# Optimization experiments

Measured on AMD Instinct MI355X. Metric: run time of the kernel, lower is better.

## Reference

```python
import jax, jax.numpy as jnp
import numpy as np

E, H, VOCAB = 32, 128, 32000
B, T = 32, 128


def _linear_params(key, out_f, in_f):
    kw, kb = jax.random.split(key)
    bound = 1.0 / np.sqrt(in_f)
    W = jax.random.uniform(kw, (out_f, in_f), jnp.float32, -bound, bound)
    b = jax.random.uniform(kb, (out_f,), jnp.float32, -bound, bound)
    return W, b


def setup_inputs() -> dict:
    key = jax.random.key(0)
    ks = jax.random.split(key, 10)
    x = jax.random.normal(ks[0], (B, T, E), jnp.float32)
    Wf, bWf = _linear_params(ks[1], H, E)
    Uf, bUf = _linear_params(ks[2], H, H)
    Wi, bWi = _linear_params(ks[3], H, E)
    Ui, bUi = _linear_params(ks[4], H, H)
    Wc, bWc = _linear_params(ks[5], H, E)
    Uc, bUc = _linear_params(ks[6], H, H)
    Wo, bWo = _linear_params(ks[7], H, E)
    Uo, bUo = _linear_params(ks[8], H, H)
    Vw, Vb = _linear_params(ks[9], VOCAB, H)
    return dict(x=x, Wf=Wf, bWf=bWf, Uf=Uf, bUf=bUf, Wi=Wi, bWi=bWi,
                Ui=Ui, bUi=bUi, Wc=Wc, bWc=bWc, Uc=Uc, bUc=bUc,
                Wo=Wo, bWo=bWo, Uo=Uo, bUo=bUo, Vw=Vw, Vb=Vb)


def _lstm_forward(x, Wf, bWf, Uf, bUf, Wi, bWi, Ui, bUi, Wc, bWc, Uc, bUc,
                  Wo, bWo, Uo, bUo, Vw, Vb):
    b = x.shape[0]
    # Precompute input-to-gate projections for all timesteps: [T, B, H] (time-major)
    xf = (jnp.einsum('bte,he->bth', x, Wf) + bWf).transpose(1, 0, 2)
    xi = (jnp.einsum('bte,he->bth', x, Wi) + bWi).transpose(1, 0, 2)
    xc = (jnp.einsum('bte,he->bth', x, Wc) + bWc).transpose(1, 0, 2)
    xo = (jnp.einsum('bte,he->bth', x, Wo) + bWo).transpose(1, 0, 2)

    h0 = jnp.zeros((b, H), x.dtype)
    c0 = jnp.zeros((b, H), x.dtype)

    def step(carry, xs):
        h, c = carry
        xf_t, xi_t, xc_t, xo_t = xs
        f = jax.nn.sigmoid(xf_t + h @ Uf.T + bUf)
        i = jax.nn.sigmoid(xi_t + h @ Ui.T + bUi)
        c_til = jnp.tanh(xc_t + h @ Uc.T + bUc)
        # Original module detaches the cell state before using it (self.ct = ct.detach())
        c_new = jax.lax.stop_gradient(f * c + i * c_til)
        o = jax.nn.sigmoid(xo_t + h @ Uo.T + bUo)
        h_new = o * jnp.tanh(c_new)
        out = h_new @ Vw.T + Vb  # [B, VOCAB]
        return (h_new, c_new), out

    (h_last, _), outs = jax.lax.scan(step, (h0, c0), (xf, xi, xc, xo))
    out_seq = outs.transpose(1, 0, 2)  # [B, T, VOCAB]
    return out_seq, h_last


def reference(x, Wf, bWf, Uf, bUf, Wi, bWi, Ui, bUi, Wc, bWc, Uc, bUc,
              Wo, bWo, Uo, bUo, Vw, Vb):
    return _lstm_forward(x, Wf, bWf, Uf, bUf, Wi, bWi, Ui, bUi, Wc, bWc,
                         Uc, bUc, Wo, bWo, Uo, bUo, Vw, Vb)
```

## Files before the change

kernel.cpp:

```cpp
#include <hip/hip_runtime.h>
#include <stdint.h>
#include <stddef.h>
#include <math.h>

#define E_ 32
#define H_ 128
#define V_ 32000
#define NB 32
#define NT 128
#define NCONS 224
#define NCHUNK 250
#define NX (NCHUNK - NCONS)
#define WSTEPS 16
#define NWIN (NT / WSTEPS)

typedef float f32x4 __attribute__((ext_vector_type(4)));
typedef short s16x8 __attribute__((ext_vector_type(8)));

__device__ inline unsigned short f2bf(float f) {
  uint32_t u = __float_as_uint(f);
  return (unsigned short)((u + 0x7FFFu + ((u >> 16) & 1u)) >> 16);
}

__global__ void zero_cnt(int* cnt) {
  if (threadIdx.x < NWIN) cnt[threadIdx.x] = 0;
}

__global__ __launch_bounds__(512, 1)
void lstm_fused(const float* __restrict__ x,
                const float* __restrict__ Wf, const float* __restrict__ bWf,
                const float* __restrict__ Uf, const float* __restrict__ bUf,
                const float* __restrict__ Wi, const float* __restrict__ bWi,
                const float* __restrict__ Ui, const float* __restrict__ bUi,
                const float* __restrict__ Wc, const float* __restrict__ bWc,
                const float* __restrict__ Uc, const float* __restrict__ bUc,
                const float* __restrict__ Wo, const float* __restrict__ bWo,
                const float* __restrict__ Uo, const float* __restrict__ bUo,
                const float* __restrict__ Vw, const float* __restrict__ Vb,
                unsigned short* __restrict__ hbf,
                int* __restrict__ cnt,
                float* __restrict__ out,
                float* __restrict__ hlast)
{
  __shared__ __align__(16) unsigned char smem[81920];
  const int bid = blockIdx.x;
  const int tid = threadIdx.x;

  if (bid < NB) {
    float* xs = reinterpret_cast<float*>(smem);
    float* hd = reinterpret_cast<float*>(smem + 16384);

    const int q  = tid & 3;
    const int jj = tid >> 2;

    const float* WL[4]  = {Wf, Wi, Wc, Wo};
    const float* UL[4]  = {Uf, Ui, Uc, Uo};
    const float* bWL[4] = {bWf, bWi, bWc, bWo};
    const float* bUL[4] = {bUf, bUi, bUc, bUo};

    f32x4 wr_[4][2];
    f32x4 ur_[4][8];
    float bias_[4];
#pragma unroll
    for (int g = 0; g < 4; ++g) {
      const f32x4* Wp = reinterpret_cast<const f32x4*>(WL[g] + jj * E_ + q * 8);
      wr_[g][0] = Wp[0]; wr_[g][1] = Wp[1];
      const f32x4* Up = reinterpret_cast<const f32x4*>(UL[g] + jj * H_ + q * 32);
#pragma unroll
      for (int r = 0; r < 8; ++r) ur_[g][r] = Up[r];
      bias_[g] = bWL[g][jj] + bUL[g][jj];
    }

    for (int i = tid; i < NT * E_; i += 512) xs[i] = x[bid * (NT * E_) + i];
    if (tid < 144) hd[tid] = 0.f;
    float creg = 0.f;
    __syncthreads();

    for (int t = 0; t < NT; ++t) {
      const int cur = t & 1, nxt = cur ^ 1;
      const f32x4* hq = reinterpret_cast<const f32x4*>(hd + cur * 144 + q * 36);
      const f32x4* xq = reinterpret_cast<const f32x4*>(xs + t * E_ + q * 8);

      f32x4 p0 = {0.f,0.f,0.f,0.f}, p1 = p0, p2 = p0, p3 = p0;
#pragma unroll
      for (int r = 0; r < 2; ++r) {
        f32x4 xv = xq[r];
        p0 += wr_[0][r] * xv; p1 += wr_[1][r] * xv;
        p2 += wr_[2][r] * xv; p3 += wr_[3][r] * xv;
      }
#pragma unroll
      for (int r = 0; r < 8; ++r) {
        f32x4 hv = hq[r];
        p0 += ur_[0][r] * hv; p1 += ur_[1][r] * hv;
        p2 += ur_[2][r] * hv; p3 += ur_[3][r] * hv;
      }
      float s0 = (p0.x + p0.y) + (p0.z + p0.w);
      float s1 = (p1.x + p1.y) + (p1.z + p1.w);
      float s2 = (p2.x + p2.y) + (p2.z + p2.w);
      float s3 = (p3.x + p3.y) + (p3.z + p3.w);
      s0 += __shfl_xor(s0, 1); s0 += __shfl_xor(s0, 2);
      s1 += __shfl_xor(s1, 1); s1 += __shfl_xor(s1, 2);
      s2 += __shfl_xor(s2, 1); s2 += __shfl_xor(s2, 2);
      s3 += __shfl_xor(s3, 1); s3 += __shfl_xor(s3, 2);
      s0 += bias_[0]; s1 += bias_[1]; s2 += bias_[2]; s3 += bias_[3];

      float own = (q == 0) ? s0 : (q == 1) ? s1 : (q == 2) ? s2 : s3;
      float xin = (q == 2) ? own + own : own;
      float sig = 1.f / (1.f + expf(-xin));
      float val = (q == 2) ? 2.f * sig - 1.f : sig;
      float v1 = __shfl_xor(val, 1);
      float v2 = __shfl_xor(val, 2);
      float v3 = __shfl_xor(v1, 2);
      float f_ = (q == 0) ? val : (q == 1) ? v1 : (q == 2) ? v2 : v3;
      float i_ = (q == 0) ? v1 : (q == 1) ? val : (q == 2) ? v3 : v2;
      float c_ = (q == 0) ? v2 : (q == 1) ? v3 : (q == 2) ? val : v1;
      float o_ = (q == 0) ? v3 : (q == 1) ? v2 : (q == 2) ? v1 : val;

      float cn = f_ * creg + i_ * c_;
      creg = cn;
      float hn = o_ * tanhf(cn);

      if (q == 0) {
        hd[nxt * 144 + jj + ((jj >> 5) << 2)] = hn;
        hbf[((size_t)t * NB + bid) * H_ + jj] = f2bf(hn);
        if (t == NT - 1) hlast[bid * H_ + jj] = hn;
      }
      __syncthreads();
      if ((t & (WSTEPS - 1)) == (WSTEPS - 1) && tid == 0)
        __hip_atomic_fetch_add(&cnt[t / WSTEPS], 1, __ATOMIC_RELEASE,
                               __HIP_MEMORY_SCOPE_AGENT);
    }
    return;
  }

  const int cid = bid - NB;
  unsigned char* vwo = smem;
  unsigned char* vwx = smem + 32768;
  unsigned char* hlb = smem + 65536;

  const int w = tid >> 6, lane = tid & 63;
  const int wr = w & 1, wc = w >> 1;
  const int l15 = lane & 15, lh = lane >> 4;

  for (int u = tid; u < 2048; u += 512) {
    int n = u >> 4, kc = u & 15;
    const f32x4* src = reinterpret_cast<const f32x4*>(
        Vw + ((size_t)(cid * 128 + n)) * H_ + kc * 8);
    f32x4 a = src[0], b = src[1];
    s16x8 o;
    o[0] = (short)f2bf(a.x); o[1] = (short)f2bf(a.y);
    o[2] = (short)f2bf(a.z); o[3] = (short)f2bf(a.w);
    o[4] = (short)f2bf(b.x); o[5] = (short)f2bf(b.y);
    o[6] = (short)f2bf(b.z); o[7] = (short)f2bf(b.w);
    *reinterpret_cast<s16x8*>(vwo + n * 256 + ((kc * 16) ^ ((n & 7) << 4))) = o;
  }
  float vbo0 = Vb[cid * 128 + wc * 32 + l15];
  float vbo1 = Vb[cid * 128 + wc * 32 + 16 + l15];
  const int hb_ = tid >> 4, hkc_ = tid & 15;
  const int hswz = hb_ * 256 + ((hkc_ * 16) ^ ((hb_ & 7) << 4));
  __syncthreads();

  for (int win = 0; win < NWIN; ++win) {
    if (tid == 0) {
      while (__hip_atomic_load(&cnt[win], __ATOMIC_RELAXED,
                               __HIP_MEMORY_SCOPE_AGENT) < NB)
        __builtin_amdgcn_s_sleep(8);
      (void)__hip_atomic_load(&cnt[win], __ATOMIC_ACQUIRE,
                              __HIP_MEMORY_SCOPE_AGENT);
    }
    __syncthreads();

    s16x8 hv = *reinterpret_cast<const s16x8*>(
        hbf + (size_t)(win * WSTEPS) * (NB * H_) + tid * 8);

    const int k = cid - NX * win;
    const bool duty = (k >= 0) && (k < NX);
    int chunk_x = NCONS + k;
    float vbx0 = 0.f, vbx1 = 0.f;
    if (duty) {
      for (int u = tid; u < 2048; u += 512) {
        int n = u >> 4, kc = u & 15;
        const f32x4* src = reinterpret_cast<const f32x4*>(
            Vw + ((size_t)(chunk_x * 128 + n)) * H_ + kc * 8);
        f32x4 a = src[0], b = src[1];
        s16x8 o;
        o[0] = (short)f2bf(a.x); o[1] = (short)f2bf(a.y);
        o[2] = (short)f2bf(a.z); o[3] = (short)f2bf(a.w);
        o[4] = (short)f2bf(b.x); o[5] = (short)f2bf(b.y);
        o[6] = (short)f2bf(b.z); o[7] = (short)f2bf(b.w);
        *reinterpret_cast<s16x8*>(vwx + n * 256 + ((kc * 16) ^ ((n & 7) << 4))) = o;
      }
      vbx0 = Vb[chunk_x * 128 + wc * 32 + l15];
      vbx1 = Vb[chunk_x * 128 + wc * 32 + 16 + l15];
    }

    for (int tt = 0; tt < WSTEPS; ++tt) {
      const int t = win * WSTEPS + tt;
      unsigned char* hcur = hlb + (tt & 1) * 8192;
      *reinterpret_cast<s16x8*>(hcur + hswz) = hv;
      if (tt < WSTEPS - 1)
        hv = *reinterpret_cast<const s16x8*>(
            hbf + (size_t)(t + 1) * (NB * H_) + tid * 8);
      __syncthreads();

      s16x8 af[4];
      const int ra = wr * 16 + l15;
#pragma unroll
      for (int kt = 0; kt < 4; ++kt)
        af[kt] = *reinterpret_cast<const s16x8*>(
            hcur + ra * 256 + ((kt * 64 + lh * 16) ^ ((ra & 7) << 4)));

      const int rb = wc * 32 + l15;
      {
        f32x4 acc0 = {0.f,0.f,0.f,0.f}, acc1 = acc0;
#pragma unroll
        for (int kt = 0; kt < 4; ++kt) {
          s16x8 b0 = *reinterpret_cast<const s16x8*>(
              vwo + rb * 256 + ((kt * 64 + lh * 16) ^ ((rb & 7) << 4)));
          s16x8 b1 = *reinterpret_cast<const s16x8*>(
              vwo + (rb + 16) * 256 + ((kt * 64 + lh * 16) ^ (((rb + 16) & 7) << 4)));
          acc0 = __builtin_amdgcn_mfma_f32_16x16x32_bf16(af[kt], b0, acc0, 0, 0, 0);
          acc1 = __builtin_amdgcn_mfma_f32_16x16x32_bf16(af[kt], b1, acc1, 0, 0, 0);
        }
        const int colbase = cid * 128 + wc * 32;
#pragma unroll
        for (int i = 0; i < 4; ++i) {
          int b = wr * 16 + lh * 4 + i;
          float* orow = out + ((size_t)b * NT + t) * V_ + colbase;
          orow[l15]      = acc0[i] + vbo0;
          orow[16 + l15] = acc1[i] + vbo1;
        }
      }
      if (duty) {
        f32x4 acc0 = {0.f,0.f,0.f,0.f}, acc1 = acc0;
#pragma unroll
        for (int kt = 0; kt < 4; ++kt) {
          s16x8 b0 = *reinterpret_cast<const s16x8*>(
              vwx + rb * 256 + ((kt * 64 + lh * 16) ^ ((rb & 7) << 4)));
          s16x8 b1 = *reinterpret_cast<const s16x8*>(
              vwx + (rb + 16) * 256 + ((kt * 64 + lh * 16) ^ (((rb + 16) & 7) << 4)));
          acc0 = __builtin_amdgcn_mfma_f32_16x16x32_bf16(af[kt], b0, acc0, 0, 0, 0);
          acc1 = __builtin_amdgcn_mfma_f32_16x16x32_bf16(af[kt], b1, acc1, 0, 0, 0);
        }
        const int colbase = chunk_x * 128 + wc * 32;
#pragma unroll
        for (int i = 0; i < 4; ++i) {
          int b = wr * 16 + lh * 4 + i;
          float* orow = out + ((size_t)b * NT + t) * V_ + colbase;
          orow[l15]      = acc0[i] + vbx0;
          orow[16 + l15] = acc1[i] + vbx1;
        }
      }
    }
  }
}

extern "C" void kernel_launch(void* const* d_in, const int* in_sizes, int n_in,
                              void* d_out, int out_size, void* d_ws, size_t ws_size,
                              hipStream_t stream) {
  const float* x   = (const float*)d_in[0];
  const float* Wf  = (const float*)d_in[1];
  const float* bWf = (const float*)d_in[2];
  const float* Uf  = (const float*)d_in[3];
  const float* bUf = (const float*)d_in[4];
  const float* Wi  = (const float*)d_in[5];
  const float* bWi = (const float*)d_in[6];
  const float* Ui  = (const float*)d_in[7];
  const float* bUi = (const float*)d_in[8];
  const float* Wc  = (const float*)d_in[9];
  const float* bWc = (const float*)d_in[10];
  const float* Uc  = (const float*)d_in[11];
  const float* bUc = (const float*)d_in[12];
  const float* Wo  = (const float*)d_in[13];
  const float* bWo = (const float*)d_in[14];
  const float* Uo  = (const float*)d_in[15];
  const float* bUo = (const float*)d_in[16];
  const float* Vw  = (const float*)d_in[17];
  const float* Vb  = (const float*)d_in[18];
  float* out = (float*)d_out;

  unsigned short* hbf = (unsigned short*)d_ws;
  int* cnt = (int*)((char*)d_ws + (1u << 20));
  float* hlast = out + (size_t)NB * NT * V_;

  hipLaunchKernelGGL(zero_cnt, dim3(1), dim3(64), 0, stream, cnt);
  hipLaunchKernelGGL(lstm_fused, dim3(256), dim3(512), 0, stream,
                     x, Wf, bWf, Uf, bUf, Wi, bWi, Ui, bUi, Wc, bWc, Uc, bUc,
                     Wo, bWo, Uo, bUo, Vw, Vb, hbf, cnt, out, hlast);
}
```

Baseline: 190.8 us.

## Double block size to 1024 threads and restructure recurrence and vocab-projection work split

Raises the workgroup size from 512 to 1024 threads. In the recurrent blocks each (hidden unit, gate) pair now gets its own pair of threads instead of four threads per unit, and fast exp/rcp intrinsics replace expf and tanhf. The bf16 h output is staged in shared memory and written once per 16-step window as packed words. In the projection blocks each wave now owns 16 output columns with one MFMA chain instead of 32, so there are more waves in flight. The aim is to shorten the serial per-step critical path and raise MFMA/store parallelism, at the cost of more register pressure at 1024 threads and small accuracy changes from the fast intrinsics.

```diff
diff --git a/kernel.cpp b/kernel.cpp
--- a/kernel.cpp
+++ b/kernel.cpp
@@ -26,7 +26,7 @@
   if (threadIdx.x < NWIN) cnt[threadIdx.x] = 0;
 }
 
-__global__ __launch_bounds__(512, 1)
+__global__ __launch_bounds__(1024, 1)
 void lstm_fused(const float* __restrict__ x,
                 const float* __restrict__ Wf, const float* __restrict__ bWf,
                 const float* __restrict__ Uf, const float* __restrict__ bUf,
@@ -47,87 +47,100 @@
   const int tid = threadIdx.x;
 
   if (bid < NB) {
-    float* xs = reinterpret_cast<float*>(smem);
-    float* hd = reinterpret_cast<float*>(smem + 16384);
-
-    const int q  = tid & 3;
-    const int jj = tid >> 2;
+    float* xs  = reinterpret_cast<float*>(smem);
+    float* hd  = reinterpret_cast<float*>(smem + 16384);
+    float* hfl = reinterpret_cast<float*>(smem + 17408);
+
+    const int j  = tid >> 3;
+    const int g  = (tid >> 1) & 3;
+    const int q2 = tid & 1;
 
     const float* WL[4]  = {Wf, Wi, Wc, Wo};
     const float* UL[4]  = {Uf, Ui, Uc, Uo};
     const float* bWL[4] = {bWf, bWi, bWc, bWo};
     const float* bUL[4] = {bUf, bUi, bUc, bUo};
 
-    f32x4 wr_[4][2];
-    f32x4 ur_[4][8];
-    float bias_[4];
-#pragma unroll
-    for (int g = 0; g < 4; ++g) {
-      const f32x4* Wp = reinterpret_cast<const f32x4*>(WL[g] + jj * E_ + q * 8);
-      wr_[g][0] = Wp[0]; wr_[g][1] = Wp[1];
-      const f32x4* Up = reinterpret_cast<const f32x4*>(UL[g] + jj * H_ + q * 32);
-#pragma unroll
-      for (int r = 0; r < 8; ++r) ur_[g][r] = Up[r];
-      bias_[g] = bWL[g][jj] + bUL[g][jj];
-    }
-
-    for (int i = tid; i < NT * E_; i += 512) xs[i] = x[bid * (NT * E_) + i];
-    if (tid < 144) hd[tid] = 0.f;
+    f32x4 ur_[16];
+    f32x4 wr_[4];
+    {
+      const f32x4* Up = reinterpret_cast<const f32x4*>(UL[g] + j * H_ + q2 * 64);
+#pragma unroll
+      for (int r = 0; r < 16; ++r) ur_[r] = Up[r];
+      const f32x4* Wp = reinterpret_cast<const f32x4*>(WL[g] + j * E_ + q2 * 16);
+#pragma unroll
+      for (int r = 0; r < 4; ++r) wr_[r] = Wp[r];
+    }
+    const float bias = bWL[g][j] + bUL[g][j];
+
+    for (int i = tid; i < NT * E_; i += 1024) xs[i] = x[bid * (NT * E_) + i];
+    if (tid < 128) { hd[tid] = 0.f; hd[128 + tid] = 0.f; }
     float creg = 0.f;
     __syncthreads();
 
-    for (int t = 0; t < NT; ++t) {
-      const int cur = t & 1, nxt = cur ^ 1;
-      const f32x4* hq = reinterpret_cast<const f32x4*>(hd + cur * 144 + q * 36);
-      const f32x4* xq = reinterpret_cast<const f32x4*>(xs + t * E_ + q * 8);
-
-      f32x4 p0 = {0.f,0.f,0.f,0.f}, p1 = p0, p2 = p0, p3 = p0;
-#pragma unroll
-      for (int r = 0; r < 2; ++r) {
-        f32x4 xv = xq[r];
-        p0 += wr_[0][r] * xv; p1 += wr_[1][r] * xv;
-        p2 += wr_[2][r] * xv; p3 += wr_[3][r] * xv;
-      }
-#pragma unroll
-      for (int r = 0; r < 8; ++r) {
-        f32x4 hv = hq[r];
-        p0 += ur_[0][r] * hv; p1 += ur_[1][r] * hv;
-        p2 += ur_[2][r] * hv; p3 += ur_[3][r] * hv;
-      }
-      float s0 = (p0.x + p0.y) + (p0.z + p0.w);
-      float s1 = (p1.x + p1.y) + (p1.z + p1.w);
-      float s2 = (p2.x + p2.y) + (p2.z + p2.w);
-      float s3 = (p3.x + p3.y) + (p3.z + p3.w);
-      s0 += __shfl_xor(s0, 1); s0 += __shfl_xor(s0, 2);
-      s1 += __shfl_xor(s1, 1); s1 += __shfl_xor(s1, 2);
-      s2 += __shfl_xor(s2, 1); s2 += __shfl_xor(s2, 2);
-      s3 += __shfl_xor(s3, 1); s3 += __shfl_xor(s3, 2);
-      s0 += bias_[0]; s1 += bias_[1]; s2 += bias_[2]; s3 += bias_[3];
-
-      float own = (q == 0) ? s0 : (q == 1) ? s1 : (q == 2) ? s2 : s3;
-      float xin = (q == 2) ? own + own : own;
-      float sig = 1.f / (1.f + expf(-xin));
-      float val = (q == 2) ? 2.f * sig - 1.f : sig;
-      float v1 = __shfl_xor(val, 1);
-      float v2 = __shfl_xor(val, 2);
-      float v3 = __shfl_xor(v1, 2);
-      float f_ = (q == 0) ? val : (q == 1) ? v1 : (q == 2) ? v2 : v3;
-      float i_ = (q == 0) ? v1 : (q == 1) ? val : (q == 2) ? v3 : v2;
-      float c_ = (q == 0) ? v2 : (q == 1) ? v3 : (q == 2) ? val : v1;
-      float o_ = (q == 0) ? v3 : (q == 1) ? v2 : (q == 2) ? v1 : val;
-
-      float cn = f_ * creg + i_ * c_;
-      creg = cn;
-      float hn = o_ * tanhf(cn);
-
-      if (q == 0) {
-        hd[nxt * 144 + jj + ((jj >> 5) << 2)] = hn;
-        hbf[((size_t)t * NB + bid) * H_ + jj] = f2bf(hn);
-        if (t == NT - 1) hlast[bid * H_ + jj] = hn;
+    for (int win = 0; win < NWIN; ++win) {
+      for (int tt = 0; tt < WSTEPS; ++tt) {
+        const int t = win * WSTEPS + tt;
+        const int cur = t & 1, nxt = cur ^ 1;
+        const f32x4* hq = reinterpret_cast<const f32x4*>(hd + cur * 128 + q2 * 64);
+        const f32x4* xq = reinterpret_cast<const f32x4*>(xs + t * E_ + q2 * 16);
+
+        f32x4 a0 = {0.f,0.f,0.f,0.f}, a1 = a0, a2 = a0, a3 = a0;
+#pragma unroll
+        for (int r = 0; r < 4; ++r) {
+          if ((r & 3) == 0) a0 += wr_[r] * xq[r];
+          else if ((r & 3) == 1) a1 += wr_[r] * xq[r];
+          else if ((r & 3) == 2) a2 += wr_[r] * xq[r];
+          else a3 += wr_[r] * xq[r];
+        }
+#pragma unroll
+        for (int r = 0; r < 16; ++r) {
+          if ((r & 3) == 0) a0 += ur_[r] * hq[r];
+          else if ((r & 3) == 1) a1 += ur_[r] * hq[r];
+          else if ((r & 3) == 2) a2 += ur_[r] * hq[r];
+          else a3 += ur_[r] * hq[r];
+        }
+        f32x4 s4 = (a0 + a1) + (a2 + a3);
+        float s = (s4.x + s4.y) + (s4.z + s4.w);
+        s += __shfl_xor(s, 1);
+        s += bias;
+
+        float xin = (g == 2) ? s + s : s;
+        float e = __expf(-xin);
+        float rv = __builtin_amdgcn_rcpf(1.f + e);
+        float val = (g == 2) ? 2.f * rv - 1.f : rv;
+
+        float v1 = __shfl_xor(val, 2);
+        float v2 = __shfl_xor(val, 4);
+        float v3 = __shfl_xor(v1, 4);
+        float f_ = (g == 0) ? val : (g == 1) ? v1 : (g == 2) ? v2 : v3;
+        float i_ = (g == 0) ? v1 : (g == 1) ? val : (g == 2) ? v3 : v2;
+        float c_ = (g == 0) ? v2 : (g == 1) ? v3 : (g == 2) ? val : v1;
+        float o_ = (g == 0) ? v3 : (g == 1) ? v2 : (g == 2) ? v1 : val;
+
+        float cn = f_ * creg + i_ * c_;
+        creg = cn;
+        float tn = 2.f * __builtin_amdgcn_rcpf(1.f + __expf(-2.f * cn)) - 1.f;
+        float hn = o_ * tn;
+
+        if ((tid & 7) == 0) {
+          hd[nxt * 128 + j] = hn;
+          hfl[tt * 128 + j] = hn;
+          if (t == NT - 1) hlast[bid * H_ + j] = hn;
+        }
+        __syncthreads();
+      }
+      {
+        const int t16 = tid >> 6;
+        const int jp  = tid & 63;
+        float f0 = hfl[t16 * 128 + jp * 2];
+        float f1 = hfl[t16 * 128 + jp * 2 + 1];
+        uint32_t pk = (uint32_t)f2bf(f0) | ((uint32_t)f2bf(f1) << 16);
+        uint32_t* hb32 = reinterpret_cast<uint32_t*>(hbf);
+        hb32[((size_t)(win * WSTEPS + t16) * NB + bid) * 64 + jp] = pk;
       }
       __syncthreads();
-      if ((t & (WSTEPS - 1)) == (WSTEPS - 1) && tid == 0)
-        __hip_atomic_fetch_add(&cnt[t / WSTEPS], 1, __ATOMIC_RELEASE,
+      if (tid == 0)
+        __hip_atomic_fetch_add(&cnt[win], 1, __ATOMIC_RELEASE,
                                __HIP_MEMORY_SCOPE_AGENT);
     }
     return;
@@ -142,7 +155,7 @@
   const int wr = w & 1, wc = w >> 1;
   const int l15 = lane & 15, lh = lane >> 4;
 
-  for (int u = tid; u < 2048; u += 512) {
+  for (int u = tid; u < 2048; u += 1024) {
     int n = u >> 4, kc = u & 15;
     const f32x4* src = reinterpret_cast<const f32x4*>(
         Vw + ((size_t)(cid * 128 + n)) * H_ + kc * 8);
@@ -154,8 +167,7 @@
     o[6] = (short)f2bf(b.z); o[7] = (short)f2bf(b.w);
     *reinterpret_cast<s16x8*>(vwo + n * 256 + ((kc * 16) ^ ((n & 7) << 4))) = o;
   }
-  float vbo0 = Vb[cid * 128 + wc * 32 + l15];
-  float vbo1 = Vb[cid * 128 + wc * 32 + 16 + l15];
+  float vbo = Vb[cid * 128 + wc * 16 + l15];
   const int hb_ = tid >> 4, hkc_ = tid & 15;
   const int hswz = hb_ * 256 + ((hkc_ * 16) ^ ((hb_ & 7) << 4));
   __syncthreads();
@@ -164,21 +176,23 @@
     if (tid == 0) {
       while (__hip_atomic_load(&cnt[win], __ATOMIC_RELAXED,
                                __HIP_MEMORY_SCOPE_AGENT) < NB)
-        __builtin_amdgcn_s_sleep(8);
+        __builtin_amdgcn_s_sleep(16);
       (void)__hip_atomic_load(&cnt[win], __ATOMIC_ACQUIRE,
                               __HIP_MEMORY_SCOPE_AGENT);
     }
     __syncthreads();
 
-    s16x8 hv = *reinterpret_cast<const s16x8*>(
-        hbf + (size_t)(win * WSTEPS) * (NB * H_) + tid * 8);
+    s16x8 hv = {};
+    if (tid < 512)
+      hv = *reinterpret_cast<const s16x8*>(
+          hbf + (size_t)(win * WSTEPS) * (NB * H_) + tid * 8);
 
     const int k = cid - NX * win;
     const bool duty = (k >= 0) && (k < NX);
     int chunk_x = NCONS + k;
-    float vbx0 = 0.f, vbx1 = 0.f;
+    float vbx = 0.f;
     if (duty) {
-      for (int u = tid; u < 2048; u += 512) {
+      for (int u = tid; u < 2048; u += 1024) {
         int n = u >> 4, kc = u & 15;
         const f32x4* src = reinterpret_cast<const f32x4*>(
             Vw + ((size_t)(chunk_x * 128 + n)) * H_ + kc * 8);
@@ -190,18 +204,18 @@
         o[6] = (short)f2bf(b.z); o[7] = (short)f2bf(b.w);
         *reinterpret_cast<s16x8*>(vwx + n * 256 + ((kc * 16) ^ ((n & 7) << 4))) = o;
       }
-      vbx0 = Vb[chunk_x * 128 + wc * 32 + l15];
-      vbx1 = Vb[chunk_x * 128 + wc * 32 + 16 + l15];
+      vbx = Vb[chunk_x * 128 + wc * 16 + l15];
     }
 
     for (int tt = 0; tt < WSTEPS; ++tt) {
       const int t = win * WSTEPS + tt;
       unsigned char* hcur = hlb + (tt & 1) * 8192;
-      *reinterpret_cast<s16x8*>(hcur + hswz) = hv;
-      if (tt < WSTEPS - 1)
+      if (tid < 512)
+        *reinterpret_cast<s16x8*>(hcur + hswz) = hv;
+      __syncthreads();
+      if (tt < WSTEPS - 1 && tid < 512)
         hv = *reinterpret_cast<const s16x8*>(
             hbf + (size_t)(t + 1) * (NB * H_) + tid * 8);
-      __syncthreads();
 
       s16x8 af[4];
       const int ra = wr * 16 + l15;
@@ -210,45 +224,35 @@
         af[kt] = *reinterpret_cast<const s16x8*>(
             hcur + ra * 256 + ((kt * 64 + lh * 16) ^ ((ra & 7) << 4)));
 
-      const int rb = wc * 32 + l15;
+      const int rb = wc * 16 + l15;
       {
-        f32x4 acc0 = {0.f,0.f,0.f,0.f}, acc1 = acc0;
+        f32x4 acc = {0.f,0.f,0.f,0.f};
 #pragma unroll
         for (int kt = 0; kt < 4; ++kt) {
           s16x8 b0 = *reinterpret_cast<const s16x8*>(
               vwo + rb * 256 + ((kt * 64 + lh * 16) ^ ((rb & 7) << 4)));
-          s16x8 b1 = *reinterpret_cast<const s16x8*>(
-              vwo + (rb + 16) * 256 + ((kt * 64 + lh * 16) ^ (((rb + 16) & 7) << 4)));
-          acc0 = __builtin_amdgcn_mfma_f32_16x16x32_bf16(af[kt], b0, acc0, 0, 0, 0);
-          acc1 = __builtin_amdgcn_mfma_f32_16x16x32_bf16(af[kt], b1, acc1, 0, 0, 0);
-        }
-        const int colbase = cid * 128 + wc * 32;
+          acc = __builtin_amdgcn_mfma_f32_16x16x32_bf16(af[kt], b0, acc, 0, 0, 0);
+        }
+        const int colbase = cid * 128 + wc * 16;
 #pragma unroll
         for (int i = 0; i < 4; ++i) {
           int b = wr * 16 + lh * 4 + i;
-          float* orow = out + ((size_t)b * NT + t) * V_ + colbase;
-          orow[l15]      = acc0[i] + vbo0;
-          orow[16 + l15] = acc1[i] + vbo1;
+          out[((size_t)b * NT + t) * V_ + colbase + l15] = acc[i] + vbo;
         }
       }
       if (duty) {
-        f32x4 acc0 = {0.f,0.f,0.f,0.f}, acc1 = acc0;
+        f32x4 acc = {0.f,0.f,0.f,0.f};
 #pragma unroll
         for (int kt = 0; kt < 4; ++kt) {
           s16x8 b0 = *reinterpret_cast<const s16x8*>(
               vwx + rb * 256 + ((kt * 64 + lh * 16) ^ ((rb & 7) << 4)));
-          s16x8 b1 = *reinterpret_cast<const s16x8*>(
-              vwx + (rb + 16) * 256 + ((kt * 64 + lh * 16) ^ (((rb + 16) & 7) << 4)));
-          acc0 = __builtin_amdgcn_mfma_f32_16x16x32_bf16(af[kt], b0, acc0, 0, 0, 0);
-          acc1 = __builtin_amdgcn_mfma_f32_16x16x32_bf16(af[kt], b1, acc1, 0, 0, 0);
-        }
-        const int colbase = chunk_x * 128 + wc * 32;
+          acc = __builtin_amdgcn_mfma_f32_16x16x32_bf16(af[kt], b0, acc, 0, 0, 0);
+        }
+        const int colbase = chunk_x * 128 + wc * 16;
 #pragma unroll
         for (int i = 0; i < 4; ++i) {
           int b = wr * 16 + lh * 4 + i;
-          float* orow = out + ((size_t)b * NT + t) * V_ + colbase;
-          orow[l15]      = acc0[i] + vbx0;
-          orow[16 + l15] = acc1[i] + vbx1;
+          out[((size_t)b * NT + t) * V_ + colbase + l15] = acc[i] + vbx;
         }
       }
     }
@@ -284,7 +288,7 @@
   float* hlast = out + (size_t)NB * NT * V_;
 
   hipLaunchKernelGGL(zero_cnt, dim3(1), dim3(64), 0, stream, cnt);
-  hipLaunchKernelGGL(lstm_fused, dim3(256), dim3(512), 0, stream,
+  hipLaunchKernelGGL(lstm_fused, dim3(256), dim3(1024), 0, stream,
                      x, Wf, bWf, Uf, bUf, Wi, bWi, Ui, bUi, Wc, bWc, Uc, bUc,
                      Wo, bWo, Uo, bUo, Vw, Vb, hbf, cnt, out, hlast);
 }
```

After: 244.8 us. +28.3%, slower.
